# Kernel tuning notes

Hardware: AMD Instinct MI355X
Metric: run time of the kernel (lower is better)

## Reference

```python
import jax, jax.numpy as jnp
import numpy as np

TOP_K = 2  # init arg top_k
EPS = 1e-9


def setup_inputs() -> dict:
    key = jax.random.key(0)
    ks = jax.random.split(key, 5)
    B, L, D, E, H, G = 2, 2048, 2048, 8, 2048, 256
    s = lambda k, sh, fan: jax.random.normal(k, sh, jnp.float32) / np.sqrt(fan)
    return {
        "x": jax.random.normal(ks[0], (B, L, D), jnp.float32),
        "wg1": s(ks[1], (D, G), D),
        "wg2": s(ks[2], (G, E), G),
        "w1": s(ks[3], (E, D, H), D),
        "w2": s(ks[4], (E, H, D), H),
    }


def reference(x, wg1, wg2, w1, w2):
    B, L, D = x.shape
    xf = x.reshape(-1, D)                                  # [T, D]
    T = xf.shape[0]

    # --- top-k gating (mlp gate) ---
    logits = jax.nn.gelu(xf @ wg1) @ wg2                   # [T, E]
    probs = jax.nn.softmax(logits, axis=-1)                # [T, E]
    top_vals, top_idx = jax.lax.top_k(probs, TOP_K)        # [T, k]
    # dense gate matrix: gate weight where expert selected, else 0
    gates = jnp.zeros_like(probs).at[jnp.arange(T)[:, None], top_idx].set(top_vals)  # [T, E]

    # --- grouped expert FFN (dense-equivalent of gather/grouped-GEMM/scatter) ---
    h = jax.nn.gelu(jnp.einsum('td,edh->teh', xf, w1))     # [T, E, H]
    gh = h * gates[:, :, None]                             # fold gates in (linear in h)
    y = jnp.einsum('teh,ehd->td', gh, w2).reshape(B, L, D)

    # --- mutual-information aux loss: -H(E) + H(E|X) ---
    p_mean = probs.mean(axis=0)                            # [E]
    loss = jnp.sum(p_mean * jnp.log(p_mean + EPS)) \
         - jnp.mean(jnp.sum(probs * jnp.log(probs + EPS), axis=-1))
    return y, loss
```

## Files before the change

kernel.cpp:

```cpp
#include <hip/hip_runtime.h>

#define T_TOK 4096
#define DDIM  2048
#define GDIM  256
#define EEXP  8
#define HDIM  2048
#define NROWS_MAX 9216
#define MAX_TILES 72

typedef float  fv4  __attribute__((ext_vector_type(4)));
typedef __bf16 bv4  __attribute__((ext_vector_type(4)));
typedef __bf16 bv8  __attribute__((ext_vector_type(8)));

#define CTRL_OFF     0
#define ROWTOK_OFF   4096
#define ROWGATE_OFF  40960
#define TOPIDX_OFF   77824
#define TOPVAL_OFF   110592
#define G_OFF        143360
#define XB_OFF       4337664
#define W1T_OFF      21114880
#define W2T_OFF      88223744
#define HBUF_OFF     155332608

struct Ctrl {
    int   counts[8];
    float psum[8];
    float entsum;
    int   ntiles;
    int   off[8];
    int   tile_e[MAX_TILES];
    int   tile_r0[MAX_TILES];
};

__device__ __forceinline__ float gelu_f(float x) {
    float x3 = x * x * x;
    return 0.5f * x * (1.0f + tanhf(0.7978845608028654f * (x + 0.044715f * x3)));
}

__device__ __forceinline__ void g2l16(const void* gptr, void* lptr) {
    __builtin_amdgcn_global_load_lds(
        (const __attribute__((address_space(1))) void*)gptr,
        (__attribute__((address_space(3))) void*)lptr, 16, 0, 0);
}

__global__ __launch_bounds__(256) void transpose_cvt(
    const float* __restrict__ w1, const float* __restrict__ w2,
    __bf16* __restrict__ w1t, __bf16* __restrict__ w2t)
{
    int b    = blockIdx.x;
    int mat  = b >> 10;
    int tile = b & 1023;
    int trow = tile >> 5, tcol = tile & 31;
    const float* src = (mat < 8) ? (w1 + (size_t)mat * 4194304)
                                 : (w2 + (size_t)(mat - 8) * 4194304);
    __bf16* dst = (mat < 8) ? (w1t + (size_t)mat * 4194304)
                            : (w2t + (size_t)(mat - 8) * 4194304);
    __shared__ float tileS[64][65];
    int tid = threadIdx.x;
    int c = tid & 63, r4 = tid >> 6;
#pragma unroll
    for (int u = 0; u < 16; u++) {
        int rr = u * 4 + r4;
        tileS[rr][c] = src[(size_t)(trow * 64 + rr) * 2048 + tcol * 64 + c];
    }
    __syncthreads();
    int c2 = (tid & 31) * 2, r8 = tid >> 5;
#pragma unroll
    for (int u = 0; u < 8; u++) {
        int rr = u * 8 + r8;
        __bf16 v0 = (__bf16)tileS[c2][rr];
        __bf16 v1 = (__bf16)tileS[c2 + 1][rr];
        size_t o = (size_t)(tcol * 64 + rr) * 2048 + trow * 64 + c2;
        dst[o]     = v0;
        dst[o + 1] = v1;
    }
}

__global__ __launch_bounds__(256) void cvt_x_kernel(const float* __restrict__ x,
                                                    __bf16* __restrict__ xb)
{
    size_t idx = ((size_t)blockIdx.x * 256 + threadIdx.x) * 4;
    fv4 v = *(const fv4*)(x + idx);
    bv4 o;
#pragma unroll
    for (int u = 0; u < 4; u++) o[u] = (__bf16)v[u];
    *(bv4*)(xb + idx) = o;
}

__global__ __launch_bounds__(256) void gating_gemm(const float* __restrict__ x,
                                                   const float* __restrict__ wg1,
                                                   float* __restrict__ g)
{
    __shared__ float As[16][68];
    __shared__ float Bs[16][68];
    int tid = threadIdx.x;
    int tx = tid & 15, ty = tid >> 4;
    int mb = blockIdx.x, nb = blockIdx.y;
    float acc[4][4];
#pragma unroll
    for (int u = 0; u < 4; u++)
#pragma unroll
        for (int v = 0; v < 4; v++) acc[u][v] = 0.f;

    int r  = tid >> 2, kq = tid & 3;
    int kb = tid >> 4, n4 = (tid & 15) * 4;
    const float* gx = x + (size_t)(mb * 64 + r) * 2048 + kq * 4;
    const float* gw = wg1 + nb * 64 + n4;

    for (int k0 = 0; k0 < 2048; k0 += 16) {
        fv4 av = *(const fv4*)(gx + k0);
        fv4 bv = *(const fv4*)(gw + (size_t)(k0 + kb) * 256);
        __syncthreads();
#pragma unroll
        for (int u = 0; u < 4; u++) As[kq * 4 + u][r] = av[u];
        *(fv4*)&Bs[kb][n4] = bv;
        __syncthreads();
#pragma unroll
        for (int k = 0; k < 16; k++) {
            fv4 a = *(const fv4*)&As[k][ty * 4];
            fv4 b = *(const fv4*)&Bs[k][tx * 4];
#pragma unroll
            for (int u = 0; u < 4; u++)
#pragma unroll
                for (int v = 0; v < 4; v++) acc[u][v] += a[u] * b[v];
        }
    }
#pragma unroll
    for (int u = 0; u < 4; u++) {
        int row = mb * 64 + ty * 4 + u;
#pragma unroll
        for (int v = 0; v < 4; v++)
            g[(size_t)row * 256 + nb * 64 + tx * 4 + v] = gelu_f(acc[u][v]);
    }
}

__global__ __launch_bounds__(256) void gate_kernel(
    const float* __restrict__ g, const float* __restrict__ wg2,
    Ctrl* __restrict__ ctrl, int* __restrict__ topidx, float* __restrict__ topval)
{
    __shared__ float wg2s[256 * 9];
    __shared__ float psum_s[8];
    __shared__ float ent_s;
    __shared__ int   cnt_s[8];
    int tid = threadIdx.x;
    for (int i = tid; i < 2048; i += 256) {
        int k = i >> 3, e = i & 7;
        wg2s[k * 9 + e] = wg2[i];
    }
    if (tid < 8) { psum_s[tid] = 0.f; cnt_s[tid] = 0; }
    if (tid == 8) ent_s = 0.f;
    __syncthreads();

    int lane = tid & 63, wv = tid >> 6;
    int t = blockIdx.x * 4 + wv;
    fv4 g4 = *(const fv4*)&g[(size_t)t * 256 + lane * 4];
    float part[8];
#pragma unroll
    for (int e = 0; e < 8; e++) part[e] = 0.f;
#pragma unroll
    for (int u = 0; u < 4; u++) {
        int k = lane * 4 + u;
        float gv = g4[u];
#pragma unroll
        for (int e = 0; e < 8; e++) part[e] += gv * wg2s[k * 9 + e];
    }
#pragma unroll
    for (int e = 0; e < 8; e++)
        for (int off = 32; off; off >>= 1) part[e] += __shfl_xor(part[e], off);

    if (lane == 0) {
        float mx = part[0];
#pragma unroll
        for (int e = 1; e < 8; e++) mx = fmaxf(mx, part[e]);
        float p[8], Z = 0.f;
#pragma unroll
        for (int e = 0; e < 8; e++) { p[e] = expf(part[e] - mx); Z += p[e]; }
        float rz = 1.f / Z;
#pragma unroll
        for (int e = 0; e < 8; e++) p[e] *= rz;
        int i0 = 0;
#pragma unroll
        for (int e = 1; e < 8; e++) if (part[e] > part[i0]) i0 = e;
        int i1 = (i0 == 0) ? 1 : 0;
#pragma unroll
        for (int e = 0; e < 8; e++)
            if (e != i0 && part[e] > part[i1]) i1 = e;
        topidx[2 * t]     = i0;
        topidx[2 * t + 1] = i1;
        topval[2 * t]     = p[i0];
        topval[2 * t + 1] = p[i1];
        float ent = 0.f;
#pragma unroll
        for (int e = 0; e < 8; e++) ent += p[e] * logf(p[e] + 1e-9f);
#pragma unroll
        for (int e = 0; e < 8; e++) atomicAdd(&psum_s[e], p[e]);
        atomicAdd(&ent_s, ent);
        atomicAdd(&cnt_s[i0], 1);
        atomicAdd(&cnt_s[i1], 1);
    }
    __syncthreads();
    if (tid < 8)                   atomicAdd(&ctrl->psum[tid], psum_s[tid]);
    else if (tid == 8)             atomicAdd(&ctrl->entsum, ent_s);
    else if (tid >= 16 && tid < 24) atomicAdd(&ctrl->counts[tid - 16], cnt_s[tid - 16]);
}

__global__ __launch_bounds__(256) void route_kernel(
    Ctrl* __restrict__ ctrl, const int* __restrict__ topidx,
    const float* __restrict__ topval, int* __restrict__ rowtok,
    float* __restrict__ rowgate)
{
    __shared__ int cur[8];
    __shared__ int offs_s[8];
    int tid = threadIdx.x;
    if (tid == 0) {
        int off = 0, nt = 0;
        for (int e = 0; e < 8; e++) {
            offs_s[e]    = off;
            ctrl->off[e] = off;
            int c = ctrl->counts[e];
            for (int m = 0; m < c; m += 128) {
                ctrl->tile_e[nt]  = e;
                ctrl->tile_r0[nt] = off + m;
                nt++;
            }
            off += ((c + 127) >> 7) << 7;
        }
        ctrl->ntiles = nt;
    }
    if (tid < 8) cur[tid] = 0;
    __syncthreads();
    for (int t = tid; t < T_TOK; t += 256) {
#pragma unroll
        for (int k = 0; k < 2; k++) {
            int e = topidx[2 * t + k];
            int p = atomicAdd(&cur[e], 1);
            int row = offs_s[e] + p;
            rowtok[row]  = t;
            rowgate[row] = topval[2 * t + k];
        }
    }
}

template <bool IS_FFN1>
__global__ __launch_bounds__(256) void gemm_grouped(
    const __bf16* __restrict__ A,
    const __bf16* __restrict__ Bt,
    const Ctrl* __restrict__ ctrl,
    const int* __restrict__ rowtok,
    const float* __restrict__ rowgate,
    __bf16* __restrict__ hbuf,
    float* __restrict__ y)
{
    int tile = blockIdx.x;
    if (tile >= ctrl->ntiles) return;
    int e  = ctrl->tile_e[tile];
    int r0 = ctrl->tile_r0[tile];
    int nb = blockIdx.y;
    const int K = 2048;

    __shared__ __bf16 As[128 * 32];
    __shared__ __bf16 Bs[128 * 32];

    int tid  = threadIdx.x;
    int lane = tid & 63, w = tid >> 6;
    int wm = w >> 1, wn = w & 1;

    int c0 = 2 * w, c1 = c0 + 1;
    int sub = lane >> 2;
    int kq  = lane & 3;
    int ra0 = c0 * 16 + sub, ra1 = c1 * 16 + sub;

    size_t gAoff0, gAoff1;
    if constexpr (IS_FFN1) {
        gAoff0 = (size_t)rowtok[r0 + ra0] * K;
        gAoff1 = (size_t)rowtok[r0 + ra1] * K;
    } else {
        gAoff0 = (size_t)(r0 + ra0) * K;
        gAoff1 = (size_t)(r0 + ra1) * K;
    }
    const __bf16* gA0 = A + gAoff0 + kq * 8;
    const __bf16* gA1 = A + gAoff1 + kq * 8;
    const __bf16* gB0 = Bt + ((size_t)e * 2048 + nb * 128 + c0 * 16 + sub) * K + kq * 8;
    const __bf16* gB1 = Bt + ((size_t)e * 2048 + nb * 128 + c1 * 16 + sub) * K + kq * 8;
    __bf16* lA0 = &As[c0 * 512];
    __bf16* lA1 = &As[c1 * 512];
    __bf16* lB0 = &Bs[c0 * 512];
    __bf16* lB1 = &Bs[c1 * 512];

    fv4 acc[4][4];
#pragma unroll
    for (int i = 0; i < 4; i++)
#pragma unroll
        for (int j = 0; j < 4; j++) acc[i][j] = (fv4)0.0f;

    int mrow = (wm * 64 + (lane & 15)) * 32 + (lane >> 4) * 8;
    int nrow = (wn * 64 + (lane & 15)) * 32 + (lane >> 4) * 8;

    for (int k0 = 0; k0 < K; k0 += 32) {
        __syncthreads();
        g2l16(gA0, lA0);
        g2l16(gA1, lA1);
        g2l16(gB0, lB0);
        g2l16(gB1, lB1);
        gA0 += 32; gA1 += 32; gB0 += 32; gB1 += 32;
        __syncthreads();
        bv8 aF[4], bF[4];
#pragma unroll
        for (int i = 0; i < 4; i++) aF[i] = *(const bv8*)&As[mrow + i * 16 * 32];
#pragma unroll
        for (int j = 0; j < 4; j++) bF[j] = *(const bv8*)&Bs[nrow + j * 16 * 32];
#pragma unroll
        for (int i = 0; i < 4; i++)
#pragma unroll
            for (int j = 0; j < 4; j++)
                acc[i][j] = __builtin_amdgcn_mfma_f32_16x16x32_bf16(aF[i], bF[j], acc[i][j], 0, 0, 0);
    }

    int col0  = nb * 128 + wn * 64 + (lane & 15);
    int rbase = wm * 64 + (lane >> 4) * 4;
#pragma unroll
    for (int i = 0; i < 4; i++) {
#pragma unroll
        for (int rr = 0; rr < 4; rr++) {
            int rglob = r0 + rbase + i * 16 + rr;
            if constexpr (IS_FFN1) {
                float gate = rowgate[rglob];
                size_t ho = (size_t)rglob * 2048;
#pragma unroll
                for (int j = 0; j < 4; j++)
                    hbuf[ho + col0 + j * 16] = (__bf16)(gelu_f(acc[i][j][rr]) * gate);
            } else {
                size_t yo = (size_t)rowtok[rglob] * 2048;
#pragma unroll
                for (int j = 0; j < 4; j++)
                    atomicAdd(&y[yo + col0 + j * 16], acc[i][j][rr]);
            }
        }
    }
}

__global__ __launch_bounds__(64) void loss_kernel(const Ctrl* __restrict__ ctrl,
                                                  float* __restrict__ out)
{
    if (threadIdx.x == 0) {
        float a = 0.f;
#pragma unroll
        for (int e = 0; e < 8; e++) {
            float pm = ctrl->psum[e] * (1.0f / 4096.0f);
            a += pm * logf(pm + 1e-9f);
        }
        out[0] = a - ctrl->entsum * (1.0f / 4096.0f);
    }
}

extern "C" void kernel_launch(void* const* d_in, const int* in_sizes, int n_in,
                              void* d_out, int out_size, void* d_ws, size_t ws_size,
                              hipStream_t stream)
{
    const float* x   = (const float*)d_in[0];
    const float* wg1 = (const float*)d_in[1];
    const float* wg2 = (const float*)d_in[2];
    const float* w1  = (const float*)d_in[3];
    const float* w2  = (const float*)d_in[4];
    float* out = (float*)d_out;

    char* ws = (char*)d_ws;
    Ctrl*   ctrl    = (Ctrl*)(ws + CTRL_OFF);
    int*    rowtok  = (int*)(ws + ROWTOK_OFF);
    float*  rowgate = (float*)(ws + ROWGATE_OFF);
    int*    topidx  = (int*)(ws + TOPIDX_OFF);
    float*  topval  = (float*)(ws + TOPVAL_OFF);
    float*  g       = (float*)(ws + G_OFF);
    __bf16* xb      = (__bf16*)(ws + XB_OFF);
    __bf16* w1t     = (__bf16*)(ws + W1T_OFF);
    __bf16* w2t     = (__bf16*)(ws + W2T_OFF);
    __bf16* hbuf    = (__bf16*)(ws + HBUF_OFF);

    hipMemsetAsync(ws + CTRL_OFF, 0, 4096, stream);
    hipMemsetAsync(ws + ROWTOK_OFF, 0, 73728, stream);
    hipMemsetAsync(d_out, 0, (size_t)out_size * sizeof(float), stream);

    transpose_cvt<<<16384, 256, 0, stream>>>(w1, w2, w1t, w2t);
    cvt_x_kernel<<<8192, 256, 0, stream>>>(x, xb);
    gating_gemm<<<dim3(64, 4), 256, 0, stream>>>(x, wg1, g);
    gate_kernel<<<1024, 256, 0, stream>>>(g, wg2, ctrl, topidx, topval);
    route_kernel<<<1, 256, 0, stream>>>(ctrl, topidx, topval, rowtok, rowgate);
    gemm_grouped<true><<<dim3(71, 16), 256, 0, stream>>>(xb, w1t, ctrl, rowtok, rowgate, hbuf, nullptr);
    gemm_grouped<false><<<dim3(71, 16), 256, 0, stream>>>(hbuf, w2t, ctrl, rowtok, rowgate, nullptr, out);
    loss_kernel<<<1, 64, 0, stream>>>(ctrl, out + 8388608);
}
```

Before: 949.0 us.

## Enlarge grouped GEMM tiles to 256x256 with swizzled LDS and XCD-aware block mapping

The grouped expert GEMMs move from 128x128 tiles with 256 threads to 256x256 tiles with 512 threads. Each wave now computes 64x128 outputs, and expert row padding becomes 256. The LDS layout gets an XOR swizzle on the k-chunk to reduce bank conflicts. A 1D grid of 320 blocks is remapped so blocks sharing a row tile are spread across XCDs. The goal is more operand reuse and less global traffic, at the cost of more padding waste, higher register pressure, and fewer blocks.

```diff
diff --git a/kernel.cpp b/kernel.cpp
--- a/kernel.cpp
+++ b/kernel.cpp
@@ -1,12 +1,8 @@
 #include <hip/hip_runtime.h>
 
 #define T_TOK 4096
-#define DDIM  2048
-#define GDIM  256
-#define EEXP  8
-#define HDIM  2048
-#define NROWS_MAX 9216
-#define MAX_TILES 72
+#define NROWS_MAX 10240
+#define MAX_TILES 40
 
 typedef float  fv4  __attribute__((ext_vector_type(4)));
 typedef __bf16 bv4  __attribute__((ext_vector_type(4)));
@@ -14,14 +10,14 @@
 
 #define CTRL_OFF     0
 #define ROWTOK_OFF   4096
-#define ROWGATE_OFF  40960
-#define TOPIDX_OFF   77824
-#define TOPVAL_OFF   110592
-#define G_OFF        143360
-#define XB_OFF       4337664
-#define W1T_OFF      21114880
-#define W2T_OFF      88223744
-#define HBUF_OFF     155332608
+#define ROWGATE_OFF  45056
+#define TOPIDX_OFF   86016
+#define TOPVAL_OFF   118784
+#define G_OFF        151552
+#define XB_OFF       4345856
+#define W1T_OFF      21123072
+#define W2T_OFF      88231936
+#define HBUF_OFF     155340800
 
 struct Ctrl {
     int   counts[8];
@@ -200,8 +196,8 @@
         atomicAdd(&cnt_s[i1], 1);
     }
     __syncthreads();
-    if (tid < 8)                   atomicAdd(&ctrl->psum[tid], psum_s[tid]);
-    else if (tid == 8)             atomicAdd(&ctrl->entsum, ent_s);
+    if (tid < 8)                    atomicAdd(&ctrl->psum[tid], psum_s[tid]);
+    else if (tid == 8)              atomicAdd(&ctrl->entsum, ent_s);
     else if (tid >= 16 && tid < 24) atomicAdd(&ctrl->counts[tid - 16], cnt_s[tid - 16]);
 }
 
@@ -219,12 +215,12 @@
             offs_s[e]    = off;
             ctrl->off[e] = off;
             int c = ctrl->counts[e];
-            for (int m = 0; m < c; m += 128) {
+            for (int m = 0; m < c; m += 256) {
                 ctrl->tile_e[nt]  = e;
                 ctrl->tile_r0[nt] = off + m;
                 nt++;
             }
-            off += ((c + 127) >> 7) << 7;
+            off += ((c + 255) >> 8) << 8;
         }
         ctrl->ntiles = nt;
     }
@@ -243,7 +239,7 @@
 }
 
 template <bool IS_FFN1>
-__global__ __launch_bounds__(256) void gemm_grouped(
+__global__ __launch_bounds__(512, 2) void gemm_grouped(
     const __bf16* __restrict__ A,
     const __bf16* __restrict__ Bt,
     const Ctrl* __restrict__ ctrl,
@@ -252,50 +248,50 @@
     __bf16* __restrict__ hbuf,
     float* __restrict__ y)
 {
-    int tile = blockIdx.x;
+    int lb   = blockIdx.x;
+    int tile = (lb & 7) * 5 + (lb >> 6);
+    int nb   = (lb >> 3) & 7;
     if (tile >= ctrl->ntiles) return;
     int e  = ctrl->tile_e[tile];
     int r0 = ctrl->tile_r0[tile];
-    int nb = blockIdx.y;
     const int K = 2048;
 
-    __shared__ __bf16 As[128 * 32];
-    __shared__ __bf16 Bs[128 * 32];
+    __shared__ __bf16 As[256 * 32];
+    __shared__ __bf16 Bs[256 * 32];
 
     int tid  = threadIdx.x;
     int lane = tid & 63, w = tid >> 6;
-    int wm = w >> 1, wn = w & 1;
+    int wr = w >> 1, wc = w & 1;
 
     int c0 = 2 * w, c1 = c0 + 1;
     int sub = lane >> 2;
-    int kq  = lane & 3;
-    int ra0 = c0 * 16 + sub, ra1 = c1 * 16 + sub;
-
-    size_t gAoff0, gAoff1;
+    int kcg = (lane & 3) ^ ((lane >> 3) & 3);
+
+    int rA0 = c0 * 16 + sub, rA1 = c1 * 16 + sub;
+    size_t ga0, ga1;
     if constexpr (IS_FFN1) {
-        gAoff0 = (size_t)rowtok[r0 + ra0] * K;
-        gAoff1 = (size_t)rowtok[r0 + ra1] * K;
+        ga0 = (size_t)rowtok[r0 + rA0] * K;
+        ga1 = (size_t)rowtok[r0 + rA1] * K;
     } else {
-        gAoff0 = (size_t)(r0 + ra0) * K;
-        gAoff1 = (size_t)(r0 + ra1) * K;
-    }
-    const __bf16* gA0 = A + gAoff0 + kq * 8;
-    const __bf16* gA1 = A + gAoff1 + kq * 8;
-    const __bf16* gB0 = Bt + ((size_t)e * 2048 + nb * 128 + c0 * 16 + sub) * K + kq * 8;
-    const __bf16* gB1 = Bt + ((size_t)e * 2048 + nb * 128 + c1 * 16 + sub) * K + kq * 8;
+        ga0 = (size_t)(r0 + rA0) * K;
+        ga1 = (size_t)(r0 + rA1) * K;
+    }
+    const __bf16* gA0 = A + ga0 + kcg * 8;
+    const __bf16* gA1 = A + ga1 + kcg * 8;
+    const __bf16* gB0 = Bt + ((size_t)e * 2048 + nb * 256 + c0 * 16 + sub) * K + kcg * 8;
+    const __bf16* gB1 = Bt + ((size_t)e * 2048 + nb * 256 + c1 * 16 + sub) * K + kcg * 8;
     __bf16* lA0 = &As[c0 * 512];
     __bf16* lA1 = &As[c1 * 512];
     __bf16* lB0 = &Bs[c0 * 512];
     __bf16* lB1 = &Bs[c1 * 512];
 
-    fv4 acc[4][4];
+    fv4 acc[4][8];
 #pragma unroll
     for (int i = 0; i < 4; i++)
 #pragma unroll
-        for (int j = 0; j < 4; j++) acc[i][j] = (fv4)0.0f;
-
-    int mrow = (wm * 64 + (lane & 15)) * 32 + (lane >> 4) * 8;
-    int nrow = (wn * 64 + (lane & 15)) * 32 + (lane >> 4) * 8;
+        for (int j = 0; j < 8; j++) acc[i][j] = (fv4)0.0f;
+
+    int frow = (lane & 15) * 32 + (((lane >> 4) ^ ((lane >> 1) & 3)) * 8);
 
     for (int k0 = 0; k0 < K; k0 += 32) {
         __syncthreads();
@@ -305,36 +301,36 @@
         g2l16(gB1, lB1);
         gA0 += 32; gA1 += 32; gB0 += 32; gB1 += 32;
         __syncthreads();
-        bv8 aF[4], bF[4];
-#pragma unroll
-        for (int i = 0; i < 4; i++) aF[i] = *(const bv8*)&As[mrow + i * 16 * 32];
-#pragma unroll
-        for (int j = 0; j < 4; j++) bF[j] = *(const bv8*)&Bs[nrow + j * 16 * 32];
+        bv8 aF[4], bF[8];
+#pragma unroll
+        for (int i = 0; i < 4; i++) aF[i] = *(const bv8*)&As[(wr * 64 + i * 16) * 32 + frow];
+#pragma unroll
+        for (int j = 0; j < 8; j++) bF[j] = *(const bv8*)&Bs[(wc * 128 + j * 16) * 32 + frow];
 #pragma unroll
         for (int i = 0; i < 4; i++)
 #pragma unroll
-            for (int j = 0; j < 4; j++)
+            for (int j = 0; j < 8; j++)
                 acc[i][j] = __builtin_amdgcn_mfma_f32_16x16x32_bf16(aF[i], bF[j], acc[i][j], 0, 0, 0);
     }
 
-    int col0  = nb * 128 + wn * 64 + (lane & 15);
-    int rbase = wm * 64 + (lane >> 4) * 4;
+    int colb = nb * 256 + wc * 128 + (lane & 15);
+    int rb   = r0 + wr * 64 + (lane >> 4) * 4;
 #pragma unroll
     for (int i = 0; i < 4; i++) {
 #pragma unroll
         for (int rr = 0; rr < 4; rr++) {
-            int rglob = r0 + rbase + i * 16 + rr;
+            int rg = rb + i * 16 + rr;
             if constexpr (IS_FFN1) {
-                float gate = rowgate[rglob];
-                size_t ho = (size_t)rglob * 2048;
-#pragma unroll
-                for (int j = 0; j < 4; j++)
-                    hbuf[ho + col0 + j * 16] = (__bf16)(gelu_f(acc[i][j][rr]) * gate);
+                float gate = rowgate[rg];
+                size_t ho = (size_t)rg * 2048;
+#pragma unroll
+                for (int j = 0; j < 8; j++)
+                    hbuf[ho + colb + j * 16] = (__bf16)(gelu_f(acc[i][j][rr]) * gate);
             } else {
-                size_t yo = (size_t)rowtok[rglob] * 2048;
-#pragma unroll
-                for (int j = 0; j < 4; j++)
-                    atomicAdd(&y[yo + col0 + j * 16], acc[i][j][rr]);
+                size_t yo = (size_t)rowtok[rg] * 2048;
+#pragma unroll
+                for (int j = 0; j < 8; j++)
+                    atomicAdd(&y[yo + colb + j * 16], acc[i][j][rr]);
             }
         }
     }
@@ -378,7 +374,7 @@
     __bf16* hbuf    = (__bf16*)(ws + HBUF_OFF);
 
     hipMemsetAsync(ws + CTRL_OFF, 0, 4096, stream);
-    hipMemsetAsync(ws + ROWTOK_OFF, 0, 73728, stream);
+    hipMemsetAsync(ws + ROWTOK_OFF, 0, 81920, stream);
     hipMemsetAsync(d_out, 0, (size_t)out_size * sizeof(float), stream);
 
     transpose_cvt<<<16384, 256, 0, stream>>>(w1, w2, w1t, w2t);
@@ -386,7 +382,7 @@
     gating_gemm<<<dim3(64, 4), 256, 0, stream>>>(x, wg1, g);
     gate_kernel<<<1024, 256, 0, stream>>>(g, wg2, ctrl, topidx, topval);
     route_kernel<<<1, 256, 0, stream>>>(ctrl, topidx, topval, rowtok, rowgate);
-    gemm_grouped<true><<<dim3(71, 16), 256, 0, stream>>>(xb, w1t, ctrl, rowtok, rowgate, hbuf, nullptr);
-    gemm_grouped<false><<<dim3(71, 16), 256, 0, stream>>>(hbuf, w2t, ctrl, rowtok, rowgate, nullptr, out);
+    gemm_grouped<true><<<320, 512, 0, stream>>>(xb, w1t, ctrl, rowtok, rowgate, hbuf, nullptr);
+    gemm_grouped<false><<<320, 512, 0, stream>>>(hbuf, w2t, ctrl, rowtok, rowgate, nullptr, out);
     loss_kernel<<<1, 64, 0, stream>>>(ctrl, out + 8388608);
 }
```

After: 957.6 us. Within noise of the previous version (+0.9%).
